# Performance work log

Measured on AMD Instinct MI355X. Metric: run time of the kernel, lower is better.

## Reference

```python
import jax, jax.numpy as jnp
import numpy as np

N, E, F_IN, HID, HEADS, C, NCLS, NG, NCONV = 50000, 800000, 128, 128, 8, 16, 10, 64, 3
EPS = 1e-5
NEG_SLOPE = 0.2


def bn_eval(x, p):
    # p: [4, dim] = (gamma, beta, running_mean, running_var); eval-mode BatchNorm1d
    g, b, m, v = p[0], p[1], p[2], p[3]
    return g * (x - m) * jax.lax.rsqrt(v + EPS) + b


def gat_conv(x, src, dst, W, a_src, a_dst, bias):
    # PyG GATConv, concat=True, add_self_loops=True, eval (no dropout)
    h = (x @ W).reshape(N, HEADS, C)                    # [N,H,C]
    alpha_s = jnp.sum(h * a_src[None], axis=-1)         # [N,H]
    alpha_d = jnp.sum(h * a_dst[None], axis=-1)         # [N,H]
    loop = jnp.arange(N)
    s = jnp.concatenate([src, loop])                    # [E+N]
    d = jnp.concatenate([dst, loop])
    logits = jax.nn.leaky_relu(alpha_s[s] + alpha_d[d], NEG_SLOPE)   # [E+N,H]
    mx = jax.lax.stop_gradient(jax.ops.segment_max(logits, d, num_segments=N))
    ex = jnp.exp(logits - mx[d])
    denom = jax.ops.segment_sum(ex, d, num_segments=N)
    alpha = ex / (denom[d] + 1e-16)                     # segment softmax over dst
    msg = h[s] * alpha[:, :, None]                      # [E+N,H,C]
    out = jax.ops.segment_sum(msg, d, num_segments=N)   # [N,H,C]
    return out.reshape(N, HEADS * C) + bias


def setup_inputs() -> dict:
    key = jax.random.key(0)
    ks = jax.random.split(key, 16)

    def bn_p(dim):
        return jnp.stack([jnp.ones(dim), jnp.full((dim,), 1e-4), jnp.zeros(dim), jnp.ones(dim)])

    sc = 0.05
    inp = {
        "x": jax.random.normal(ks[0], (N, F_IN), jnp.float32),
        "edge_index": jax.random.randint(ks[1], (2, E), 0, N),
        "batch": jnp.sort(jax.random.randint(ks[2], (N,), 0, NG)),
        "bn_feat_params": bn_p(F_IN),
        "w_feat": jax.random.normal(ks[3], (F_IN, HID), jnp.float32) * sc,
        "b_feat": jnp.zeros((HID,), jnp.float32),
        "bns_conv_params": jnp.stack([bn_p(HID)] * NCONV),
        "gat_w": jax.random.normal(ks[4], (NCONV, HID, HID), jnp.float32) * sc,
        "gat_att_src": jax.random.normal(ks[5], (NCONV, HEADS, C), jnp.float32) * sc,
        "gat_att_dst": jax.random.normal(ks[6], (NCONV, HEADS, C), jnp.float32) * sc,
        "gat_b": jnp.zeros((NCONV, HID), jnp.float32),
        "bns_fc_params": jnp.stack([bn_p(HID)] * 1),
        "fc_w": jax.random.normal(ks[7], (1, HID, HID), jnp.float32) * sc,
        "fc_b": jnp.zeros((1, HID), jnp.float32),
        "bn_hidden_params": bn_p(HID),
        "w_class": jax.random.normal(ks[8], (HID, NCLS), jnp.float32) * sc,
        "b_class": jnp.zeros((NCLS,), jnp.float32),
    }
    return inp


def reference(x, edge_index, batch, bn_feat_params, w_feat, b_feat, bns_conv_params,
              gat_w, gat_att_src, gat_att_dst, gat_b, bns_fc_params, fc_w, fc_b,
              bn_hidden_params, w_class, b_class):
    src, dst = edge_index[0], edge_index[1]
    h = bn_eval(x, bn_feat_params)
    h = jax.nn.relu(h @ w_feat + b_feat)             # GCNConv(gfn=True) == linear
    for i in range(NCONV):
        h = bn_eval(h, bns_conv_params[i])
        h = jax.nn.relu(gat_conv(h, src, dst, gat_w[i], gat_att_src[i], gat_att_dst[i], gat_b[i]))
    g = jax.ops.segment_sum(h, batch, num_segments=NG)   # global_add_pool -> [NG,HID]
    for i in range(fc_w.shape[0]):
        g = jax.nn.relu(bn_eval(g, bns_fc_params[i]) @ fc_w[i] + fc_b[i])
    g = bn_eval(g, bn_hidden_params)
    logits = g @ w_class + b_class
    return jax.nn.log_softmax(logits, axis=-1)
```

## Files before the change

### kernel.cpp

```cpp
#include <hip/hip_runtime.h>

#define NN 50000
#define E_EDGES 800000
#define F_INN 128
#define HIDD 128
#define HEADS 8
#define CDIM 16
#define NCLS 10
#define NGG 64
#define NCONV 3
#define EPSS 1e-5f
#define NEG_SLOPE 0.2f

#define WROWS 144
#define WSTRIDE (WROWS * 128)
#define BSTRIDE 144

#define BSH 7
#define BSZ 128
#define NB ((NN + BSZ - 1) / BSZ)
#define STAGE_CAP 16
#define BIN_BLOCKS 256
#define BIN_CHUNK (E_EDGES / BIN_BLOCKS)
#define SORT_BUF 4608
#define BUCKET_PAD 896
#define PW_KCH 32
#define GTILES ((NN + 127) / 128)

typedef __attribute__((ext_vector_type(8))) short short8;
typedef __attribute__((ext_vector_type(4))) float f32x4;
typedef __attribute__((ext_vector_type(2))) float f32x2;

__device__ __forceinline__ float lrelu(float x) { return x > 0.f ? x : NEG_SLOPE * x; }

__device__ __forceinline__ float bf2f(ushort u) {
    union { unsigned int i; float f; } v;
    v.i = ((unsigned int)u) << 16;
    return v.f;
}
__device__ __forceinline__ ushort f2bf(float f) {
    union { float f; unsigned int i; } v;
    v.f = f;
    unsigned int r = (v.i + 0x7fffu + ((v.i >> 16) & 1u)) >> 16;
    return (ushort)r;
}
__device__ __forceinline__ unsigned char f2fp8(float f) {
    int r = __builtin_amdgcn_cvt_pk_fp8_f32(f, f, 0, false);
    return (unsigned char)(r & 0xff);
}

__global__ __launch_bounds__(256) void prep_all(
    const float* __restrict__ bn_feat, const float* __restrict__ w_feat,
    const float* __restrict__ b_feat, const float* __restrict__ bns_conv,
    const float* __restrict__ gat_w, const float* __restrict__ att_src,
    const float* __restrict__ att_dst, const int* __restrict__ dst,
    ushort* __restrict__ Wt, float* __restrict__ bp, int* __restrict__ bcnt)
{
    __shared__ __align__(16) char smem[18560];
    int blk = blockIdx.x;
    int t = threadIdx.x;

    if (blk < 16) {
        float* Wl = (float*)smem;
        float* aak = Wl + PW_KCH * 129;
        int layer = blk >> 2;
        int k0 = (blk & 3) * PW_KCH;
        const float* bn; const float* W;
        if (layer == 0) { bn = bn_feat; W = w_feat; }
        else { bn = bns_conv + (layer - 1) * 4 * HIDD; W = gat_w + (size_t)(layer - 1) * HIDD * HIDD; }
        if (t < PW_KCH) {
            int k = k0 + t;
            aak[t] = bn[k] * rsqrtf(bn[3 * HIDD + k] + EPSS);
        }
        for (int i = t; i < PW_KCH * 128; i += 256) {
            int kk = i >> 7, n = i & 127;
            Wl[kk * 129 + n] = W[(size_t)(k0 + kk) * 128 + n];
        }
        __syncthreads();
        ushort* wrow = Wt + (size_t)layer * WSTRIDE;
        for (int i = t; i < 128 * PW_KCH; i += 256) {
            int n = i >> 5, kk = i & 31;
            wrow[n * 128 + k0 + kk] = f2bf(aak[kk] * Wl[kk * 129 + n]);
        }
    } else if (blk < 20) {
        float* ccs = (float*)smem;
        int layer = blk - 16;
        const float* bn; const float* W;
        if (layer == 0) { bn = bn_feat; W = w_feat; }
        else { bn = bns_conv + (layer - 1) * 4 * HIDD; W = gat_w + (size_t)(layer - 1) * HIDD * HIDD; }
        if (t < 128) {
            float a = bn[t] * rsqrtf(bn[3 * HIDD + t] + EPSS);
            ccs[t] = bn[HIDD + t] - bn[2 * HIDD + t] * a;
        }
        __syncthreads();
        if (t < 128) {
            float bacc = (layer == 0) ? b_feat[t] : 0.f;
            for (int k = 0; k < 128; ++k) bacc += ccs[k] * W[(size_t)k * 128 + t];
            bp[layer * BSTRIDE + t] = bacc;
        }
    } else if (blk < 23) {
        float* Wl   = (float*)smem;
        float* redS = (float*)(smem + 16512);
        float* redD = redS + 256;
        int li = blk - 20;
        int L = li + 1;
        const float* bn = bns_conv + li * 4 * HIDD;
        const float* W  = gat_w + (size_t)li * HIDD * HIDD;
        const float* as = att_src + li * HEADS * CDIM;
        const float* ad = att_dst + li * HEADS * CDIM;
        ushort* Wo = Wt + (size_t)L * WSTRIDE;
        int kl = t >> 3, h = t & 7;
        float acc_s = 0.f, acc_d = 0.f;
        for (int c0 = 0; c0 < 4; ++c0) {
            int k0 = c0 * 32;
            __syncthreads();
            for (int i = t; i < 32 * 128; i += 256) {
                int kk = i >> 7, n = i & 127;
                Wl[kk * 129 + n] = W[(size_t)(k0 + kk) * 128 + n];
            }
            __syncthreads();
            int k = k0 + kl;
            float a  = bn[k] * rsqrtf(bn[3 * HIDD + k] + EPSS);
            float cc = bn[HIDD + k] - bn[2 * HIDD + k] * a;
            float ps = 0.f, pd = 0.f;
            #pragma unroll
            for (int c = 0; c < 16; ++c) {
                float wv = Wl[kl * 129 + h * 16 + c];
                ps += wv * as[h * 16 + c];
                pd += wv * ad[h * 16 + c];
            }
            Wo[(128 + h) * 128 + k] = f2bf(a * ps);
            Wo[(136 + h) * 128 + k] = f2bf(a * pd);
            acc_s += cc * ps;
            acc_d += cc * pd;
        }
        redS[t] = acc_s; redD[t] = acc_d;
        __syncthreads();
        if (t < 8) {
            float s = 0.f, d = 0.f;
            for (int q = 0; q < 32; ++q) { s += redS[q * 8 + t]; d += redD[q * 8 + t]; }
            bp[L * BSTRIDE + 128 + t] = s;
            bp[L * BSTRIDE + 136 + t] = d;
        }
    } else {
        int* hh = (int*)smem;
        for (int i = t; i < NB; i += 256) hh[i] = 0;
        __syncthreads();
        int cblk = blk - 23;
        for (int e = cblk * 256 + t; e < E_EDGES; e += 256 * 256)
            atomicAdd(&hh[dst[e] >> BSH], 1);
        __syncthreads();
        for (int i = t; i < NB; i += 256)
            if (hh[i]) atomicAdd(&bcnt[i], hh[i]);
    }
}

__global__ __launch_bounds__(512) void bucket_scan(const int* __restrict__ bcnt,
    int* __restrict__ bbase_pad, int* __restrict__ bpos, int* __restrict__ bout)
{
    __shared__ int s2[512], s3[512];
    int t = threadIdx.x;
    int c = (t < NB) ? bcnt[t] : 0;
    int p = (c + 15) & ~15;
    int q = (c + BUCKET_PAD + 7) & ~7;
    s2[t] = p; s3[t] = q;
    __syncthreads();
    for (int d = 1; d < 512; d <<= 1) {
        int a2 = (t >= d) ? s2[t - d] : 0;
        int a3 = (t >= d) ? s3[t - d] : 0;
        __syncthreads();
        s2[t] += a2; s3[t] += a3;
        __syncthreads();
    }
    if (t < NB) {
        int b2 = s2[t] - p;
        bbase_pad[t] = b2;
        bpos[t] = b2;
        bout[t] = s3[t] - q;
    }
}

__global__ __launch_bounds__(256) void bin_edges(const int* __restrict__ src,
    const int* __restrict__ dst, int* __restrict__ bpos, unsigned int* __restrict__ tmp)
{
    __shared__ unsigned int stage[NB * STAGE_CAP];
    __shared__ int scnt[NB];
    int t = threadIdx.x;
    for (int i = t; i < NB; i += 256) scnt[i] = 0;
    __syncthreads();
    int cbeg = blockIdx.x * BIN_CHUNK;
    int cend = cbeg + BIN_CHUNK;
    for (int tb = cbeg; tb < cend; tb += 256) {
        int e = tb + t;
        if (e < cend) {
            int d = dst[e];
            int b = d >> BSH;
            unsigned int pk = ((unsigned int)(d & (BSZ - 1)) << 16) | (unsigned int)src[e];
            int slot = atomicAdd(&scnt[b], 1);
            if (slot < STAGE_CAP) stage[b * STAGE_CAP + slot] = pk;
            else { int g = atomicAdd(&bpos[b], 1); tmp[g] = pk; }
        }
        __syncthreads();
        for (int b = t; b < NB; b += 256) {
            if (scnt[b] >= STAGE_CAP) {
                int g = atomicAdd(&bpos[b], STAGE_CAP);
                #pragma unroll
                for (int j = 0; j < STAGE_CAP; ++j) tmp[g + j] = stage[b * STAGE_CAP + j];
                scnt[b] = 0;
            }
        }
        __syncthreads();
    }
    for (int b = t; b < NB; b += 256) {
        int n = scnt[b];
        if (n > 0) {
            int g = atomicAdd(&bpos[b], n);
            for (int j = 0; j < n; ++j) tmp[g + j] = stage[b * STAGE_CAP + j];
        }
    }
}

__global__ __launch_bounds__(256) void bucket_sort(const int* __restrict__ bcnt,
    const int* __restrict__ bbase_pad, const int* __restrict__ bout,
    const unsigned int* __restrict__ tmp, ushort* __restrict__ csr,
    unsigned int* __restrict__ rowptr)
{
    __shared__ unsigned int buf[SORT_BUF];
    __shared__ int hist[BSZ];
    __shared__ int pex[BSZ];
    __shared__ int cur[BSZ];
    int b = blockIdx.x, t = threadIdx.x;
    int m = bcnt[b];
    if (m > SORT_BUF) m = SORT_BUF;
    int base_in = bbase_pad[b], base_out = bout[b];
    if (t < BSZ) hist[t] = 0;
    __syncthreads();
    for (int i = t; i < m; i += 256) {
        unsigned int pk = tmp[base_in + i];
        buf[i] = pk;
        atomicAdd(&hist[pk >> 16], 1);
    }
    __syncthreads();
    int pd = 0;
    if (t < BSZ) { pd = (hist[t] + 7) & ~7; pex[t] = pd; }
    __syncthreads();
    for (int d = 1; d < BSZ; d <<= 1) {
        int a = (t < BSZ && t >= d) ? pex[t - d] : 0;
        __syncthreads();
        if (t < BSZ) pex[t] += a;
        __syncthreads();
    }
    if (t < BSZ) {
        int ex = pex[t] - pd;
        pex[t] = ex;
        cur[t] = ex;
        int node = b * BSZ + t;
        if (node < NN)
            rowptr[node] = (unsigned int)(base_out + ex) | ((unsigned int)hist[t] << 21);
    }
    __syncthreads();
    for (int i = t; i < m; i += 256) {
        unsigned int pk = buf[i];
        int dl = pk >> 16;
        int p = atomicAdd(&cur[dl], 1);
        csr[base_out + p] = (ushort)(pk & 0xffffu);
    }
    __syncthreads();
    if (t < BSZ) {
        int ex = pex[t], hn = hist[t], pdn = (hn + 7) & ~7;
        for (int i = hn; i < pdn; ++i) csr[base_out + ex + i] = 0;
    }
}

template <int F32IN, int ALPHAS>
__global__ __launch_bounds__(256) void gemm_mfma(const void* __restrict__ Ain,
    const ushort* __restrict__ Wt, const float* __restrict__ bias,
    ushort* __restrict__ Out, unsigned char* __restrict__ h8,
    float* __restrict__ alph_s, float* __restrict__ alph_d, int n, int dorelu)
{
    const int NT = ALPHAS ? 9 : 8;
    int t = threadIdx.x;
    int wave = t >> 6, lane = t & 63;
    int m16 = lane & 15, quad = lane >> 4;
    int rbase = blockIdx.x * 128 + wave * 32;

    short8 afrag[2][4];
    #pragma unroll
    for (int tt = 0; tt < 2; ++tt) {
        int arow_i = rbase + tt * 16 + m16;
        size_t arow = (size_t)(arow_i < n ? arow_i : 0) * HIDD + quad * 8;
        if (F32IN) {
            const float* ap = (const float*)Ain + arow;
            #pragma unroll
            for (int kk = 0; kk < 4; ++kk) {
                float4 lo = *(const float4*)(ap + kk * 32);
                float4 hi = *(const float4*)(ap + kk * 32 + 4);
                short8 f;
                f[0] = (short)f2bf(lo.x); f[1] = (short)f2bf(lo.y);
                f[2] = (short)f2bf(lo.z); f[3] = (short)f2bf(lo.w);
                f[4] = (short)f2bf(hi.x); f[5] = (short)f2bf(hi.y);
                f[6] = (short)f2bf(hi.z); f[7] = (short)f2bf(hi.w);
                afrag[tt][kk] = f;
            }
        } else {
            const ushort* ap = (const ushort*)Ain + arow;
            #pragma unroll
            for (int kk = 0; kk < 4; ++kk)
                afrag[tt][kk] = *(const short8*)(ap + kk * 32);
        }
    }

    f32x4 acc[2][9];
    #pragma unroll
    for (int tt = 0; tt < 2; ++tt)
        #pragma unroll
        for (int nt = 0; nt < NT; ++nt) acc[tt][nt] = (f32x4){0.f, 0.f, 0.f, 0.f};

    #pragma unroll
    for (int nt = 0; nt < NT; ++nt) {
        const ushort* brow = Wt + (size_t)(nt * 16 + m16) * HIDD + quad * 8;
        #pragma unroll
        for (int kk = 0; kk < 4; ++kk) {
            short8 bfrag = *(const short8*)(brow + kk * 32);
            acc[0][nt] = __builtin_amdgcn_mfma_f32_16x16x32_bf16(afrag[0][kk], bfrag, acc[0][nt], 0, 0, 0);
            acc[1][nt] = __builtin_amdgcn_mfma_f32_16x16x32_bf16(afrag[1][kk], bfrag, acc[1][nt], 0, 0, 0);
        }
    }

    #pragma unroll
    for (int tt = 0; tt < 2; ++tt) {
        int tb = rbase + tt * 16;
        #pragma unroll
        for (int nt = 0; nt < 8; ++nt) {
            int col = nt * 16 + m16;
            float bv = bias[col];
            #pragma unroll
            for (int r = 0; r < 4; ++r) {
                int orow = tb + quad * 4 + r;
                if (orow < n) {
                    float v = acc[tt][nt][r] + bv;
                    if (dorelu) v = fmaxf(v, 0.f);
                    Out[(size_t)orow * HIDD + col] = f2bf(v);
                    if (ALPHAS) h8[(size_t)orow * HIDD + col] = f2fp8(v);
                }
            }
        }
        if (ALPHAS) {
            float bv = bias[128 + m16];
            #pragma unroll
            for (int r = 0; r < 4; ++r) {
                int orow = tb + quad * 4 + r;
                if (orow < n) {
                    float v = acc[tt][8][r] + bv;
                    if (m16 < 8) alph_s[orow * HEADS + m16] = v;
                    else         alph_d[orow * HEADS + (m16 - 8)] = v;
                }
            }
        }
    }
}

__global__ __launch_bounds__(256) void gat_aggregate(
    const ushort* __restrict__ h, const unsigned char* __restrict__ h8,
    const float* __restrict__ as, const float* __restrict__ ad,
    const unsigned int* __restrict__ rowptr, const ushort* __restrict__ csr,
    const float* __restrict__ bias, ushort* __restrict__ out)
{
    int wid = (blockIdx.x * 256 + threadIdx.x) >> 6;
    int v = __builtin_amdgcn_readfirstlane(wid);
    if (v >= NN) return;
    int lane = threadIdx.x & 63;
    int hd = lane >> 3;
    int slot = lane & 7;
    int gbase = lane & ~7;
    unsigned int rp = rowptr[v];
    int beg = rp & 0x1FFFFF;
    int cnt = rp >> 21;
    float adv = ad[v * HEADS + hd];

    const unsigned int* h32 = (const unsigned int*)h;
    const ushort* h8v = (const ushort*)h8;

    float wself = __expf(lrelu(as[v * HEADS + hd] + adv));
    unsigned int hv = h32[(size_t)v * 64 + lane];
    float acc0 = wself * bf2f((ushort)(hv & 0xffff));
    float acc1 = wself * bf2f((ushort)(hv >> 16));
    float wsum_own = 0.f;

    int ngro = (cnt + 7) >> 3;
    if (ngro > 0) {
        const uint4* epk = (const uint4*)(csr + beg);
        int u0[8], u1[8];
        float l_own0, l_own1;
        unsigned int x0[8], x1[8];
        {
            uint4 pk = epk[0];
            u0[0] = pk.x & 0xffff; u0[1] = pk.x >> 16;
            u0[2] = pk.y & 0xffff; u0[3] = pk.y >> 16;
            u0[4] = pk.z & 0xffff; u0[5] = pk.z >> 16;
            u0[6] = pk.w & 0xffff; u0[7] = pk.w >> 16;
            unsigned int d = slot < 4 ? (slot < 2 ? pk.x : pk.y)
                                      : (slot < 6 ? pk.z : pk.w);
            int u_own = (slot & 1) ? (int)(d >> 16) : (int)(d & 0xffff);
            l_own0 = as[u_own * HEADS + hd];
            #pragma unroll
            for (int j = 0; j < 8; ++j) x0[j] = h8v[(size_t)u0[j] * 64 + lane];
        }
        for (int g = 0; g < ngro; ++g) {
            bool more = (g + 1 < ngro);
            if (more) {
                uint4 pk = epk[g + 1];
                u1[0] = pk.x & 0xffff; u1[1] = pk.x >> 16;
                u1[2] = pk.y & 0xffff; u1[3] = pk.y >> 16;
                u1[4] = pk.z & 0xffff; u1[5] = pk.z >> 16;
                u1[6] = pk.w & 0xffff; u1[7] = pk.w >> 16;
                unsigned int d = slot < 4 ? (slot < 2 ? pk.x : pk.y)
                                          : (slot < 6 ? pk.z : pk.w);
                int u_own = (slot & 1) ? (int)(d >> 16) : (int)(d & 0xffff);
                l_own1 = as[u_own * HEADS + hd];
                #pragma unroll
                for (int j = 0; j < 8; ++j) x1[j] = h8v[(size_t)u1[j] * 64 + lane];
            }
            float w_own = __expf(lrelu(l_own0 + adv));
            if (g * 8 + slot >= cnt) w_own = 0.f;
            wsum_own += w_own;
            #pragma unroll
            for (int j = 0; j < 8; ++j) {
                float wj = __shfl(w_own, gbase + j, 64);
                f32x2 hv2 = __builtin_amdgcn_cvt_pk_f32_fp8((int)x0[j], false);
                acc0 += wj * hv2[0];
                acc1 += wj * hv2[1];
            }
            if (more) {
                l_own0 = l_own1;
                #pragma unroll
                for (int j = 0; j < 8; ++j) { u0[j] = u1[j]; x0[j] = x1[j]; }
            }
        }
    }

    #pragma unroll
    for (int off = 1; off < 8; off <<= 1) wsum_own += __shfl_xor(wsum_own, off);
    float denom = wself + wsum_own;

    float inv = 1.f / (denom + 1e-16f);
    int c = 2 * lane;
    float o0 = fmaxf(acc0 * inv + bias[c], 0.f);
    float o1 = fmaxf(acc1 * inv + bias[c + 1], 0.f);
    ((unsigned int*)out)[(size_t)v * 64 + lane] =
        (unsigned int)f2bf(o0) | ((unsigned int)f2bf(o1) << 16);
}

__global__ __launch_bounds__(256) void pool_head(const ushort* __restrict__ h,
    const int* __restrict__ batch,
    const float* __restrict__ bns_fc, const float* __restrict__ fc_w,
    const float* __restrict__ fc_b, const float* __restrict__ bn_hid,
    const float* __restrict__ w_class, const float* __restrict__ b_class,
    float* __restrict__ out)
{
    __shared__ float sred[256];
    __shared__ float v1[HIDD];
    __shared__ float v2[HIDD];
    __shared__ float lg[NCLS];
    __shared__ float lse;
    __shared__ int bounds[2];
    int gb = blockIdx.x, t = threadIdx.x;

    if (t < 2) {
        int key = gb + t;
        int lo = 0, hi = NN;
        while (lo < hi) {
            int mid = (lo + hi) >> 1;
            if (batch[mid] < key) lo = mid + 1; else hi = mid;
        }
        bounds[t] = lo;
    }
    __syncthreads();
    int beg = bounds[0], end = bounds[1];

    int half = t >> 7, c = t & 127;
    float a0 = 0.f, a1 = 0.f, a2 = 0.f, a3 = 0.f;
    int r = beg + half;
    for (; r + 6 < end; r += 8) {
        a0 += bf2f(h[(size_t)r * HIDD + c]);
        a1 += bf2f(h[(size_t)(r + 2) * HIDD + c]);
        a2 += bf2f(h[(size_t)(r + 4) * HIDD + c]);
        a3 += bf2f(h[(size_t)(r + 6) * HIDD + c]);
    }
    for (; r < end; r += 2) a0 += bf2f(h[(size_t)r * HIDD + c]);
    sred[t] = (a0 + a1) + (a2 + a3);
    __syncthreads();

    if (t < HIDD) {
        float gv = sred[t] + sred[t + 128];
        float gamma = bns_fc[t], beta = bns_fc[HIDD + t];
        float mu = bns_fc[2 * HIDD + t], var = bns_fc[3 * HIDD + t];
        v1[t] = (gv - mu) * gamma * rsqrtf(var + EPSS) + beta;
    }
    __syncthreads();

    if (t < HIDD) {
        float acc = fc_b[t];
        for (int k = 0; k < HIDD; ++k) acc += v1[k] * fc_w[k * HIDD + t];
        acc = fmaxf(acc, 0.f);
        float gamma = bn_hid[t], beta = bn_hid[HIDD + t];
        float mu = bn_hid[2 * HIDD + t], var = bn_hid[3 * HIDD + t];
        v2[t] = (acc - mu) * gamma * rsqrtf(var + EPSS) + beta;
    }
    __syncthreads();

    if (t < NCLS) {
        float acc2 = b_class[t];
        for (int k = 0; k < HIDD; ++k) acc2 += v2[k] * w_class[k * NCLS + t];
        lg[t] = acc2;
    }
    __syncthreads();
    if (t == 0) {
        float mx = lg[0];
        for (int i = 1; i < NCLS; ++i) mx = fmaxf(mx, lg[i]);
        float ss = 0.f;
        for (int i = 0; i < NCLS; ++i) ss += __expf(lg[i] - mx);
        lse = mx + __logf(ss);
    }
    __syncthreads();
    if (t < NCLS) out[gb * NCLS + t] = lg[t] - lse;
}

extern "C" void kernel_launch(void* const* d_in, const int* in_sizes, int n_in,
                              void* d_out, int out_size, void* d_ws, size_t ws_size,
                              hipStream_t stream)
{
    const float* x        = (const float*)d_in[0];
    const int*   edge     = (const int*)d_in[1];
    const int*   batch    = (const int*)d_in[2];
    const float* bn_feat  = (const float*)d_in[3];
    const float* w_feat   = (const float*)d_in[4];
    const float* b_feat   = (const float*)d_in[5];
    const float* bns_conv = (const float*)d_in[6];
    const float* gat_w    = (const float*)d_in[7];
    const float* att_src  = (const float*)d_in[8];
    const float* att_dst  = (const float*)d_in[9];
    const float* gat_b    = (const float*)d_in[10];
    const float* bns_fc   = (const float*)d_in[11];
    const float* fc_w     = (const float*)d_in[12];
    const float* fc_b     = (const float*)d_in[13];
    const float* bn_hid   = (const float*)d_in[14];
    const float* w_class  = (const float*)d_in[15];
    const float* b_class  = (const float*)d_in[16];
    float* out = (float*)d_out;
    (void)in_sizes; (void)n_in; (void)out_size; (void)ws_size;

    char* ws = (char*)d_ws;
    size_t off = 0;
    auto alloc = [&](size_t bytes) {
        void* p = ws + off;
        off = (off + bytes + 255) & ~(size_t)255;
        return p;
    };
    ushort* Wt        = (ushort*)alloc((size_t)4 * WSTRIDE * sizeof(ushort));
    float*  bp        = (float*)alloc(4 * BSTRIDE * sizeof(float));
    ushort* h_a       = (ushort*)alloc((size_t)NN * HIDD * sizeof(ushort));
    ushort* h_b       = (ushort*)alloc((size_t)NN * HIDD * sizeof(ushort));
    unsigned char* h8 = (unsigned char*)alloc((size_t)NN * HIDD);
    float*  alph_s    = (float*)alloc((size_t)NN * HEADS * sizeof(float));
    float*  alph_d    = (float*)alloc((size_t)NN * HEADS * sizeof(float));
    int*    bcnt      = (int*)alloc(NB * sizeof(int));
    int*    bbase_pad = (int*)alloc(NB * sizeof(int));
    int*    bpos      = (int*)alloc(NB * sizeof(int));
    int*    bout      = (int*)alloc(NB * sizeof(int));
    unsigned int* tmp = (unsigned int*)alloc((size_t)(E_EDGES + NB * STAGE_CAP) * sizeof(unsigned int));
    unsigned int* rowptr = (unsigned int*)alloc((size_t)NN * sizeof(unsigned int));
    ushort* csr       = (ushort*)alloc((size_t)(E_EDGES + NB * BUCKET_PAD + 16) * sizeof(ushort));

    const int* src = edge;
    const int* dst = edge + E_EDGES;

    hipMemsetAsync(bcnt, 0, NB * sizeof(int), stream);
    prep_all<<<279, 256, 0, stream>>>(bn_feat, w_feat, b_feat, bns_conv, gat_w,
                                      att_src, att_dst, dst, Wt, bp, bcnt);
    bucket_scan<<<1, 512, 0, stream>>>(bcnt, bbase_pad, bpos, bout);
    bin_edges<<<BIN_BLOCKS, 256, 0, stream>>>(src, dst, bpos, tmp);
    bucket_sort<<<NB, 256, 0, stream>>>(bcnt, bbase_pad, bout, tmp, csr, rowptr);

    gemm_mfma<1, 0><<<GTILES, 256, 0, stream>>>(x, Wt, bp, h_a,
        nullptr, nullptr, nullptr, NN, 1);

    for (int i = 0; i < NCONV; ++i) {
        gemm_mfma<0, 1><<<GTILES, 256, 0, stream>>>(h_a,
            Wt + (size_t)(i + 1) * WSTRIDE, bp + (i + 1) * BSTRIDE, h_b, h8,
            alph_s, alph_d, NN, 0);
        gat_aggregate<<<(NN + 3) / 4, 256, 0, stream>>>(h_b, h8, alph_s, alph_d,
                                                        rowptr, csr, gat_b + i * HIDD, h_a);
    }

    pool_head<<<NGG, 256, 0, stream>>>(h_a, batch, bns_fc, fc_w, fc_b, bn_hid,
                                       w_class, b_class, out);
}
```

Before: 353.4 us.

## Merge CSR build into fewer launches with per-block local binning tables

Replaces the global histogram, scan, atomic binning and bucket sort pipeline with a two-kernel scheme. Each binning block sorts its own edge chunk locally by bucket in shared memory and writes a per-block offset table. The sort kernel gathers the chunk segments for its bucket and is fused with the first input-projection GEMM in one launch. This removes the memset, the single-block scan kernel and global atomics, and makes the CSR use fixed-capacity buckets (edges beyond capacity are truncated) plus a strided table read.

```diff
diff --git a/kernel.cpp b/kernel.cpp
--- a/kernel.cpp
+++ b/kernel.cpp
@@ -19,11 +19,11 @@
 #define BSH 7
 #define BSZ 128
 #define NB ((NN + BSZ - 1) / BSZ)
-#define STAGE_CAP 16
 #define BIN_BLOCKS 256
 #define BIN_CHUNK (E_EDGES / BIN_BLOCKS)
+#define TABW 392
+#define CAPB 4608
 #define SORT_BUF 4608
-#define BUCKET_PAD 896
 #define PW_KCH 32
 #define GTILES ((NN + 127) / 128)
 
@@ -49,12 +49,101 @@
     return (unsigned char)(r & 0xff);
 }
 
-__global__ __launch_bounds__(256) void prep_all(
+template <int F32IN, int ALPHAS>
+__device__ __forceinline__ void gemm_core(int tile, int t,
+    const void* __restrict__ Ain, const ushort* __restrict__ Wt,
+    const float* __restrict__ bias, ushort* __restrict__ Out,
+    unsigned char* __restrict__ h8, float* __restrict__ alph_s,
+    float* __restrict__ alph_d, int n, int dorelu)
+{
+    const int NT = ALPHAS ? 9 : 8;
+    int wave = t >> 6, lane = t & 63;
+    int m16 = lane & 15, quad = lane >> 4;
+    int rbase = tile * 128 + wave * 32;
+
+    short8 afrag[2][4];
+    #pragma unroll
+    for (int tt = 0; tt < 2; ++tt) {
+        int arow_i = rbase + tt * 16 + m16;
+        size_t arow = (size_t)(arow_i < n ? arow_i : 0) * HIDD + quad * 8;
+        if (F32IN) {
+            const float* ap = (const float*)Ain + arow;
+            #pragma unroll
+            for (int kk = 0; kk < 4; ++kk) {
+                float4 lo = *(const float4*)(ap + kk * 32);
+                float4 hi = *(const float4*)(ap + kk * 32 + 4);
+                short8 f;
+                f[0] = (short)f2bf(lo.x); f[1] = (short)f2bf(lo.y);
+                f[2] = (short)f2bf(lo.z); f[3] = (short)f2bf(lo.w);
+                f[4] = (short)f2bf(hi.x); f[5] = (short)f2bf(hi.y);
+                f[6] = (short)f2bf(hi.z); f[7] = (short)f2bf(hi.w);
+                afrag[tt][kk] = f;
+            }
+        } else {
+            const ushort* ap = (const ushort*)Ain + arow;
+            #pragma unroll
+            for (int kk = 0; kk < 4; ++kk)
+                afrag[tt][kk] = *(const short8*)(ap + kk * 32);
+        }
+    }
+
+    f32x4 acc[2][9];
+    #pragma unroll
+    for (int tt = 0; tt < 2; ++tt)
+        #pragma unroll
+        for (int nt = 0; nt < NT; ++nt) acc[tt][nt] = (f32x4){0.f, 0.f, 0.f, 0.f};
+
+    #pragma unroll
+    for (int nt = 0; nt < NT; ++nt) {
+        const ushort* brow = Wt + (size_t)(nt * 16 + m16) * HIDD + quad * 8;
+        #pragma unroll
+        for (int kk = 0; kk < 4; ++kk) {
+            short8 bfrag = *(const short8*)(brow + kk * 32);
+            acc[0][nt] = __builtin_amdgcn_mfma_f32_16x16x32_bf16(afrag[0][kk], bfrag, acc[0][nt], 0, 0, 0);
+            acc[1][nt] = __builtin_amdgcn_mfma_f32_16x16x32_bf16(afrag[1][kk], bfrag, acc[1][nt], 0, 0, 0);
+        }
+    }
+
+    #pragma unroll
+    for (int tt = 0; tt < 2; ++tt) {
+        int tb = rbase + tt * 16;
+        #pragma unroll
+        for (int nt = 0; nt < 8; ++nt) {
+            int col = nt * 16 + m16;
+            float bv = bias[col];
+            #pragma unroll
+            for (int r = 0; r < 4; ++r) {
+                int orow = tb + quad * 4 + r;
+                if (orow < n) {
+                    float v = acc[tt][nt][r] + bv;
+                    if (dorelu) v = fmaxf(v, 0.f);
+                    Out[(size_t)orow * HIDD + col] = f2bf(v);
+                    if (ALPHAS) h8[(size_t)orow * HIDD + col] = f2fp8(v);
+                }
+            }
+        }
+        if (ALPHAS) {
+            float bv = bias[128 + m16];
+            #pragma unroll
+            for (int r = 0; r < 4; ++r) {
+                int orow = tb + quad * 4 + r;
+                if (orow < n) {
+                    float v = acc[tt][8][r] + bv;
+                    if (m16 < 8) alph_s[orow * HEADS + m16] = v;
+                    else         alph_d[orow * HEADS + (m16 - 8)] = v;
+                }
+            }
+        }
+    }
+}
+
+__global__ __launch_bounds__(256) void prep_bin(
     const float* __restrict__ bn_feat, const float* __restrict__ w_feat,
     const float* __restrict__ b_feat, const float* __restrict__ bns_conv,
     const float* __restrict__ gat_w, const float* __restrict__ att_src,
-    const float* __restrict__ att_dst, const int* __restrict__ dst,
-    ushort* __restrict__ Wt, float* __restrict__ bp, int* __restrict__ bcnt)
+    const float* __restrict__ att_dst, const int* __restrict__ src,
+    const int* __restrict__ dst, ushort* __restrict__ Wt,
+    float* __restrict__ bp, unsigned int* __restrict__ tmp, int* __restrict__ tab)
 {
     __shared__ __align__(16) char smem[18560];
     int blk = blockIdx.x;
@@ -143,221 +232,130 @@
             bp[L * BSTRIDE + 136 + t] = d;
         }
     } else {
-        int* hh = (int*)smem;
-        for (int i = t; i < NB; i += 256) hh[i] = 0;
-        __syncthreads();
-        int cblk = blk - 23;
-        for (int e = cblk * 256 + t; e < E_EDGES; e += 256 * 256)
-            atomicAdd(&hh[dst[e] >> BSH], 1);
-        __syncthreads();
-        for (int i = t; i < NB; i += 256)
-            if (hh[i]) atomicAdd(&bcnt[i], hh[i]);
-    }
-}
-
-__global__ __launch_bounds__(512) void bucket_scan(const int* __restrict__ bcnt,
-    int* __restrict__ bbase_pad, int* __restrict__ bpos, int* __restrict__ bout)
-{
-    __shared__ int s2[512], s3[512];
-    int t = threadIdx.x;
-    int c = (t < NB) ? bcnt[t] : 0;
-    int p = (c + 15) & ~15;
-    int q = (c + BUCKET_PAD + 7) & ~7;
-    s2[t] = p; s3[t] = q;
-    __syncthreads();
-    for (int d = 1; d < 512; d <<= 1) {
-        int a2 = (t >= d) ? s2[t - d] : 0;
-        int a3 = (t >= d) ? s3[t - d] : 0;
-        __syncthreads();
-        s2[t] += a2; s3[t] += a3;
-        __syncthreads();
-    }
-    if (t < NB) {
-        int b2 = s2[t] - p;
-        bbase_pad[t] = b2;
-        bpos[t] = b2;
-        bout[t] = s3[t] - q;
-    }
-}
-
-__global__ __launch_bounds__(256) void bin_edges(const int* __restrict__ src,
-    const int* __restrict__ dst, int* __restrict__ bpos, unsigned int* __restrict__ tmp)
-{
-    __shared__ unsigned int stage[NB * STAGE_CAP];
-    __shared__ int scnt[NB];
-    int t = threadIdx.x;
-    for (int i = t; i < NB; i += 256) scnt[i] = 0;
-    __syncthreads();
-    int cbeg = blockIdx.x * BIN_CHUNK;
-    int cend = cbeg + BIN_CHUNK;
-    for (int tb = cbeg; tb < cend; tb += 256) {
-        int e = tb + t;
-        if (e < cend) {
+        unsigned int* stage = (unsigned int*)smem;
+        int* hist = (int*)(smem + 12512);
+        int* A    = hist + TABW;
+        int k = blk - 23;
+        int cbeg = k * BIN_CHUNK;
+        int cend = cbeg + BIN_CHUNK;
+
+        for (int i = t; i < TABW; i += 256) hist[i] = 0;
+        __syncthreads();
+        for (int e = cbeg + t; e < cend; e += 256)
+            atomicAdd(&hist[dst[e] >> BSH], 1);
+        __syncthreads();
+        int i1 = t + 256;
+        int c0 = hist[t];
+        int c1 = (i1 < TABW) ? hist[i1] : 0;
+        A[t] = c0; A[i1] = c1;
+        __syncthreads();
+        for (int d = 1; d < 512; d <<= 1) {
+            int a0 = (t >= d) ? A[t - d] : 0;
+            int a1 = A[i1 - d];
+            __syncthreads();
+            A[t] += a0; A[i1] += a1;
+            __syncthreads();
+        }
+        int e0 = A[t] - c0;
+        int e1 = A[i1] - c1;
+        tab[(size_t)k * TABW + t] = e0;
+        if (i1 < TABW) tab[(size_t)k * TABW + i1] = e1;
+        hist[t] = e0;
+        if (i1 < TABW) hist[i1] = e1;
+        __syncthreads();
+        for (int e = cbeg + t; e < cend; e += 256) {
             int d = dst[e];
             int b = d >> BSH;
             unsigned int pk = ((unsigned int)(d & (BSZ - 1)) << 16) | (unsigned int)src[e];
-            int slot = atomicAdd(&scnt[b], 1);
-            if (slot < STAGE_CAP) stage[b * STAGE_CAP + slot] = pk;
-            else { int g = atomicAdd(&bpos[b], 1); tmp[g] = pk; }
-        }
-        __syncthreads();
-        for (int b = t; b < NB; b += 256) {
-            if (scnt[b] >= STAGE_CAP) {
-                int g = atomicAdd(&bpos[b], STAGE_CAP);
-                #pragma unroll
-                for (int j = 0; j < STAGE_CAP; ++j) tmp[g + j] = stage[b * STAGE_CAP + j];
-                scnt[b] = 0;
-            }
-        }
-        __syncthreads();
-    }
-    for (int b = t; b < NB; b += 256) {
-        int n = scnt[b];
-        if (n > 0) {
-            int g = atomicAdd(&bpos[b], n);
-            for (int j = 0; j < n; ++j) tmp[g + j] = stage[b * STAGE_CAP + j];
-        }
-    }
-}
-
-__global__ __launch_bounds__(256) void bucket_sort(const int* __restrict__ bcnt,
-    const int* __restrict__ bbase_pad, const int* __restrict__ bout,
-    const unsigned int* __restrict__ tmp, ushort* __restrict__ csr,
-    unsigned int* __restrict__ rowptr)
-{
-    __shared__ unsigned int buf[SORT_BUF];
-    __shared__ int hist[BSZ];
-    __shared__ int pex[BSZ];
-    __shared__ int cur[BSZ];
-    int b = blockIdx.x, t = threadIdx.x;
-    int m = bcnt[b];
-    if (m > SORT_BUF) m = SORT_BUF;
-    int base_in = bbase_pad[b], base_out = bout[b];
-    if (t < BSZ) hist[t] = 0;
-    __syncthreads();
-    for (int i = t; i < m; i += 256) {
-        unsigned int pk = tmp[base_in + i];
-        buf[i] = pk;
-        atomicAdd(&hist[pk >> 16], 1);
-    }
-    __syncthreads();
-    int pd = 0;
-    if (t < BSZ) { pd = (hist[t] + 7) & ~7; pex[t] = pd; }
-    __syncthreads();
-    for (int d = 1; d < BSZ; d <<= 1) {
-        int a = (t < BSZ && t >= d) ? pex[t - d] : 0;
-        __syncthreads();
-        if (t < BSZ) pex[t] += a;
-        __syncthreads();
-    }
-    if (t < BSZ) {
-        int ex = pex[t] - pd;
-        pex[t] = ex;
-        cur[t] = ex;
-        int node = b * BSZ + t;
-        if (node < NN)
-            rowptr[node] = (unsigned int)(base_out + ex) | ((unsigned int)hist[t] << 21);
-    }
-    __syncthreads();
-    for (int i = t; i < m; i += 256) {
-        unsigned int pk = buf[i];
-        int dl = pk >> 16;
-        int p = atomicAdd(&cur[dl], 1);
-        csr[base_out + p] = (ushort)(pk & 0xffffu);
-    }
-    __syncthreads();
-    if (t < BSZ) {
-        int ex = pex[t], hn = hist[t], pdn = (hn + 7) & ~7;
-        for (int i = hn; i < pdn; ++i) csr[base_out + ex + i] = 0;
-    }
-}
-
-template <int F32IN, int ALPHAS>
-__global__ __launch_bounds__(256) void gemm_mfma(const void* __restrict__ Ain,
+            int p = atomicAdd(&hist[b], 1);
+            stage[p] = pk;
+        }
+        __syncthreads();
+        for (int i = t; i < BIN_CHUNK; i += 256)
+            tmp[(size_t)k * BIN_CHUNK + i] = stage[i];
+    }
+}
+
+__global__ __launch_bounds__(256) void sort_gemm0(
+    const int* __restrict__ tab, const unsigned int* __restrict__ tmp,
+    ushort* __restrict__ csr, unsigned int* __restrict__ rowptr,
+    const float* __restrict__ x, const ushort* __restrict__ Wt,
+    const float* __restrict__ bp, ushort* __restrict__ h_a)
+{
+    int t = threadIdx.x;
+    if (blockIdx.x < NB) {
+        __shared__ unsigned int buf[SORT_BUF];
+        __shared__ int sc[256];
+        __shared__ int o0s[256];
+        __shared__ int hist[BSZ], pex[BSZ], cur[BSZ];
+        int b = blockIdx.x;
+        int base_out = b * CAPB;
+
+        int o0 = tab[(size_t)t * TABW + b];
+        int o1 = tab[(size_t)t * TABW + b + 1];
+        int c = o1 - o0;
+        o0s[t] = o0;
+        sc[t] = c;
+        __syncthreads();
+        for (int d = 1; d < 256; d <<= 1) {
+            int a = (t >= d) ? sc[t - d] : 0;
+            __syncthreads();
+            sc[t] += a;
+            __syncthreads();
+        }
+        int m = sc[255];
+        int mybase = sc[t] - c;
+        if (m > CAPB - BSZ * 7) m = CAPB - BSZ * 7;
+        for (int j = 0; j < c; ++j) {
+            int p = mybase + j;
+            if (p < m) buf[p] = tmp[(size_t)t * BIN_CHUNK + o0s[t] + j];
+        }
+        if (t < BSZ) hist[t] = 0;
+        __syncthreads();
+        for (int i = t; i < m; i += 256) atomicAdd(&hist[buf[i] >> 16], 1);
+        __syncthreads();
+        int pd = 0;
+        if (t < BSZ) { pd = (hist[t] + 7) & ~7; pex[t] = pd; }
+        __syncthreads();
+        for (int d = 1; d < BSZ; d <<= 1) {
+            int a = (t < BSZ && t >= d) ? pex[t - d] : 0;
+            __syncthreads();
+            if (t < BSZ) pex[t] += a;
+            __syncthreads();
+        }
+        if (t < BSZ) {
+            int ex = pex[t] - pd;
+            pex[t] = ex;
+            cur[t] = ex;
+            int node = b * BSZ + t;
+            if (node < NN)
+                rowptr[node] = (unsigned int)(base_out + ex) | ((unsigned int)hist[t] << 21);
+        }
+        __syncthreads();
+        for (int i = t; i < m; i += 256) {
+            unsigned int pk = buf[i];
+            int dl = pk >> 16;
+            int p = atomicAdd(&cur[dl], 1);
+            csr[base_out + p] = (ushort)(pk & 0xffffu);
+        }
+        __syncthreads();
+        if (t < BSZ) {
+            int ex = pex[t], hn = hist[t], pdn = (hn + 7) & ~7;
+            for (int i = hn; i < pdn; ++i) csr[base_out + ex + i] = 0;
+        }
+    } else {
+        gemm_core<1, 0>(blockIdx.x - NB, t, x, Wt, bp, h_a,
+                        nullptr, nullptr, nullptr, NN, 1);
+    }
+}
+
+__global__ __launch_bounds__(256) void gemm_conv(const ushort* __restrict__ Ain,
     const ushort* __restrict__ Wt, const float* __restrict__ bias,
     ushort* __restrict__ Out, unsigned char* __restrict__ h8,
-    float* __restrict__ alph_s, float* __restrict__ alph_d, int n, int dorelu)
-{
-    const int NT = ALPHAS ? 9 : 8;
-    int t = threadIdx.x;
-    int wave = t >> 6, lane = t & 63;
-    int m16 = lane & 15, quad = lane >> 4;
-    int rbase = blockIdx.x * 128 + wave * 32;
-
-    short8 afrag[2][4];
-    #pragma unroll
-    for (int tt = 0; tt < 2; ++tt) {
-        int arow_i = rbase + tt * 16 + m16;
-        size_t arow = (size_t)(arow_i < n ? arow_i : 0) * HIDD + quad * 8;
-        if (F32IN) {
-            const float* ap = (const float*)Ain + arow;
-            #pragma unroll
-            for (int kk = 0; kk < 4; ++kk) {
-                float4 lo = *(const float4*)(ap + kk * 32);
-                float4 hi = *(const float4*)(ap + kk * 32 + 4);
-                short8 f;
-                f[0] = (short)f2bf(lo.x); f[1] = (short)f2bf(lo.y);
-                f[2] = (short)f2bf(lo.z); f[3] = (short)f2bf(lo.w);
-                f[4] = (short)f2bf(hi.x); f[5] = (short)f2bf(hi.y);
-                f[6] = (short)f2bf(hi.z); f[7] = (short)f2bf(hi.w);
-                afrag[tt][kk] = f;
-            }
-        } else {
-            const ushort* ap = (const ushort*)Ain + arow;
-            #pragma unroll
-            for (int kk = 0; kk < 4; ++kk)
-                afrag[tt][kk] = *(const short8*)(ap + kk * 32);
-        }
-    }
-
-    f32x4 acc[2][9];
-    #pragma unroll
-    for (int tt = 0; tt < 2; ++tt)
-        #pragma unroll
-        for (int nt = 0; nt < NT; ++nt) acc[tt][nt] = (f32x4){0.f, 0.f, 0.f, 0.f};
-
-    #pragma unroll
-    for (int nt = 0; nt < NT; ++nt) {
-        const ushort* brow = Wt + (size_t)(nt * 16 + m16) * HIDD + quad * 8;
-        #pragma unroll
-        for (int kk = 0; kk < 4; ++kk) {
-            short8 bfrag = *(const short8*)(brow + kk * 32);
-            acc[0][nt] = __builtin_amdgcn_mfma_f32_16x16x32_bf16(afrag[0][kk], bfrag, acc[0][nt], 0, 0, 0);
-            acc[1][nt] = __builtin_amdgcn_mfma_f32_16x16x32_bf16(afrag[1][kk], bfrag, acc[1][nt], 0, 0, 0);
-        }
-    }
-
-    #pragma unroll
-    for (int tt = 0; tt < 2; ++tt) {
-        int tb = rbase + tt * 16;
-        #pragma unroll
-        for (int nt = 0; nt < 8; ++nt) {
-            int col = nt * 16 + m16;
-            float bv = bias[col];
-            #pragma unroll
-            for (int r = 0; r < 4; ++r) {
-                int orow = tb + quad * 4 + r;
-                if (orow < n) {
-                    float v = acc[tt][nt][r] + bv;
-                    if (dorelu) v = fmaxf(v, 0.f);
-                    Out[(size_t)orow * HIDD + col] = f2bf(v);
-                    if (ALPHAS) h8[(size_t)orow * HIDD + col] = f2fp8(v);
-                }
-            }
-        }
-        if (ALPHAS) {
-            float bv = bias[128 + m16];
-            #pragma unroll
-            for (int r = 0; r < 4; ++r) {
-                int orow = tb + quad * 4 + r;
-                if (orow < n) {
-                    float v = acc[tt][8][r] + bv;
-                    if (m16 < 8) alph_s[orow * HEADS + m16] = v;
-                    else         alph_d[orow * HEADS + (m16 - 8)] = v;
-                }
-            }
-        }
-    }
+    float* __restrict__ alph_s, float* __restrict__ alph_d)
+{
+    gemm_core<0, 1>(blockIdx.x, threadIdx.x, Ain, Wt, bias, Out, h8,
+                    alph_s, alph_d, NN, 0);
 }
 
 __global__ __launch_bounds__(256) void gat_aggregate(
@@ -564,31 +562,23 @@
     unsigned char* h8 = (unsigned char*)alloc((size_t)NN * HIDD);
     float*  alph_s    = (float*)alloc((size_t)NN * HEADS * sizeof(float));
     float*  alph_d    = (float*)alloc((size_t)NN * HEADS * sizeof(float));
-    int*    bcnt      = (int*)alloc(NB * sizeof(int));
-    int*    bbase_pad = (int*)alloc(NB * sizeof(int));
-    int*    bpos      = (int*)alloc(NB * sizeof(int));
-    int*    bout      = (int*)alloc(NB * sizeof(int));
-    unsigned int* tmp = (unsigned int*)alloc((size_t)(E_EDGES + NB * STAGE_CAP) * sizeof(unsigned int));
+    int*    tab       = (int*)alloc((size_t)BIN_BLOCKS * TABW * sizeof(int));
+    unsigned int* tmp = (unsigned int*)alloc((size_t)E_EDGES * sizeof(unsigned int));
     unsigned int* rowptr = (unsigned int*)alloc((size_t)NN * sizeof(unsigned int));
-    ushort* csr       = (ushort*)alloc((size_t)(E_EDGES + NB * BUCKET_PAD + 16) * sizeof(ushort));
+    ushort* csr       = (ushort*)alloc((size_t)NB * CAPB * sizeof(ushort) + 64);
 
     const int* src = edge;
     const int* dst = edge + E_EDGES;
 
-    hipMemsetAsync(bcnt, 0, NB * sizeof(int), stream);
-    prep_all<<<279, 256, 0, stream>>>(bn_feat, w_feat, b_feat, bns_conv, gat_w,
-                                      att_src, att_dst, dst, Wt, bp, bcnt);
-    bucket_scan<<<1, 512, 0, stream>>>(bcnt, bbase_pad, bpos, bout);
-    bin_edges<<<BIN_BLOCKS, 256, 0, stream>>>(src, dst, bpos, tmp);
-    bucket_sort<<<NB, 256, 0, stream>>>(bcnt, bbase_pad, bout, tmp, csr, rowptr);
-
-    gemm_mfma<1, 0><<<GTILES, 256, 0, stream>>>(x, Wt, bp, h_a,
-        nullptr, nullptr, nullptr, NN, 1);
+    prep_bin<<<279, 256, 0, stream>>>(bn_feat, w_feat, b_feat, bns_conv, gat_w,
+                                      att_src, att_dst, src, dst, Wt, bp, tmp, tab);
+    sort_gemm0<<<NB + GTILES, 256, 0, stream>>>(tab, tmp, csr, rowptr,
+                                                x, Wt, bp, h_a);
 
     for (int i = 0; i < NCONV; ++i) {
-        gemm_mfma<0, 1><<<GTILES, 256, 0, stream>>>(h_a,
+        gemm_conv<<<GTILES, 256, 0, stream>>>(h_a,
             Wt + (size_t)(i + 1) * WSTRIDE, bp + (i + 1) * BSTRIDE, h_b, h8,
-            alph_s, alph_d, NN, 0);
+            alph_s, alph_d);
         gat_aggregate<<<(NN + 3) / 4, 256, 0, stream>>>(h_b, h8, alph_s, alph_d,
                                                         rowptr, csr, gat_b + i * HIDD, h_a);
     }
```

Measured after the change: 326.0 us. 7.8% less time.
